# Optimization experiments

Hardware: AMD Instinct MI355X
Metric: run time of the kernel (lower is better)

The kernel has to match this reference:

```python
import jax, jax.numpy as jnp
import numpy as np

N = 8192
LATENT_DIM = 64


def setup_inputs() -> dict:
    key = jax.random.key(0)
    kx, ky = jax.random.split(key)
    x = jax.random.normal(kx, (N, LATENT_DIM), dtype=jnp.float32)
    y = jax.random.normal(ky, (N, LATENT_DIM), dtype=jnp.float32)
    return {"x": x, "y": y}


def _rbf_kernel(a, b):
    # Faithful to torch: exp(-mean((a_i - b_j)^2, axis=dim) / dim)
    #                  = exp(-||a_i - b_j||^2 / dim^2)
    # Computed via the expanded-sq-dist identity to avoid the [N, N, dim]
    # tiled intermediate the torch code materializes.
    dim = a.shape[1]
    sq_a = jnp.sum(a * a, axis=1)  # [Na]
    sq_b = jnp.sum(b * b, axis=1)  # [Nb]
    sq_dist = sq_a[:, None] + sq_b[None, :] - 2.0 * (a @ b.T)  # [Na, Nb]
    return jnp.exp(-sq_dist / (dim * dim))


def reference(x, y):
    # MMD with RBF kernel: mean k(x,x) + mean k(y,y) - 2 mean k(x,y)
    kxx = jnp.mean(_rbf_kernel(x, x))
    kyy = jnp.mean(_rbf_kernel(y, y))
    kxy = jnp.mean(_rbf_kernel(x, y))
    return kxx + kyy - 2.0 * kxy
```

## Files before the change

### kernel.cpp

```cpp
#include <hip/hip_runtime.h>
#include <cmath>

#define NPTS 8192
#define DIM 64
#define BT 128
#define KSTR 132

#define LEAF_F   0
#define LEAF_N   (3 * 8192 * 64)
#define ROWS_F   (LEAF_F + LEAF_N)
#define ROWS_N   (3 * 8192)
#define MEANS_F  (ROWS_F + ROWS_N)
#define NX_F     ((MEANS_F + 3 + 3) & ~3)
#define NY_F     (NX_F + 8192)
#define SPLIT_F  (NY_F + 8192)
#define SPLIT_ELEMS (NPTS * DIM)


typedef short bf16x8 __attribute__((ext_vector_type(8)));
typedef float f32x4  __attribute__((ext_vector_type(4)));

__device__ __forceinline__ unsigned short f32_bf16_rne(float f) {
    unsigned u = __float_as_uint(f);
    return (unsigned short)((u + 0x7FFFu + ((u >> 16) & 1u)) >> 16);
}
__device__ __forceinline__ float bf16_f32(unsigned short h) {
    return __uint_as_float(((unsigned)h) << 16);
}

__global__ void prep_kernel(const float* __restrict__ x, const float* __restrict__ y,
                            unsigned short* __restrict__ Xh, unsigned short* __restrict__ Xl,
                            unsigned short* __restrict__ Yh, unsigned short* __restrict__ Yl,
                            float* __restrict__ nx, float* __restrict__ ny) {
    int r = blockIdx.x * 256 + threadIdx.x;
    int isY = r >= NPTS;
    int rr = isY ? r - NPTS : r;
    const float4* Rg = (const float4*)((isY ? y : x) + (size_t)rr * DIM);
    unsigned short* Hh = isY ? Yh : Xh;
    unsigned short* Hl = isY ? Yl : Xl;
    const int t16 = rr >> 4, mrow = rr & 15;
    float s = 0.f;
    #pragma unroll
    for (int k4 = 0; k4 < 16; ++k4) {
        float4 v = Rg[k4];
        ushort4 h, l;
        h.x = f32_bf16_rne(v.x); l.x = f32_bf16_rne(v.x - bf16_f32(h.x));
        h.y = f32_bf16_rne(v.y); l.y = f32_bf16_rne(v.y - bf16_f32(h.y));
        h.z = f32_bf16_rne(v.z); l.z = f32_bf16_rne(v.z - bf16_f32(h.z));
        h.w = f32_bf16_rne(v.w); l.w = f32_bf16_rne(v.w - bf16_f32(h.w));
        int off = t16 * 1024 + (k4 >> 3) * 512 + ((k4 >> 1) & 3) * 128 + mrow * 8 + (k4 & 1) * 4;
        *(ushort4*)(Hh + off) = h;
        *(ushort4*)(Hl + off) = l;
        s = fmaf(v.x, v.x, s); s = fmaf(v.y, v.y, s);
        s = fmaf(v.z, v.z, s); s = fmaf(v.w, v.w, s);
    }
    if (isY) ny[rr] = s; else nx[rr] = s;
}

__global__ __launch_bounds__(512, 4) void mmd_tile_kernel(
    const unsigned short* __restrict__ Xh, const unsigned short* __restrict__ Xl,
    const unsigned short* __restrict__ Yh, const unsigned short* __restrict__ Yl,
    const float* __restrict__ nx, const float* __restrict__ ny,
    float* __restrict__ leafs)
{
    const int gi = blockIdx.x;
    const int gj = blockIdx.y;
    int zz, bx, by;
    if (blockIdx.z == 1) {
        if (gi >= 64) return;
        zz = 2; bx = gi; by = gj;
    } else if (gi > gj) {
        zz = 0; by = gj; bx = gi - 1;
    } else {
        zz = 1; by = gi; bx = gj;
    }

    __shared__ float Ks[128 * KSTR];
    __shared__ float sqA[BT];
    __shared__ float sqB[BT];

    const int t = threadIdx.x;
    const size_t arow = (size_t)by * BT;
    const size_t brow = (size_t)bx * BT;
    const int cb = bx;

    const unsigned short* pAh = (zz == 1) ? Yh : Xh;
    const unsigned short* pAl = (zz == 1) ? Yl : Xl;
    const unsigned short* pBh = (zz == 0) ? Xh : Yh;
    const unsigned short* pBl = (zz == 0) ? Xl : Yl;

    if (t < 256) {
        const float* nA = (zz == 1) ? ny : nx;
        const float* nB = (zz == 0) ? nx : ny;
        if (t < BT) sqA[t] = nA[arow + t];
        else        sqB[t - BT] = nB[brow + t - BT];
    }
    __syncthreads();

    const int lane = t & 63;
    const int wv   = t >> 6;
    const int mrow = lane & 15;
    const int quad = lane >> 4;
    const int rblk = (wv & 3) << 5;
    const int cblk = (wv >> 2) << 6;

    const int aT = by * 8 + (wv & 3) * 2;
    const int bT = bx * 8 + (wv >> 2) * 4;
    const int lsub = quad * 128 + mrow * 8;

    bf16x8 fAh[2][2], fAl[2][2];
    #pragma unroll
    for (int rt = 0; rt < 2; ++rt)
        #pragma unroll
        for (int kc = 0; kc < 2; ++kc) {
            int off = (aT + rt) * 1024 + kc * 512 + lsub;
            fAh[rt][kc] = *(const bf16x8*)(pAh + off);
            fAl[rt][kc] = *(const bf16x8*)(pAl + off);
        }

    f32x4 acc[2][4];
    #pragma unroll
    for (int rt = 0; rt < 2; ++rt)
        #pragma unroll
        for (int ct = 0; ct < 4; ++ct)
            acc[rt][ct] = (f32x4){0.f, 0.f, 0.f, 0.f};

    #pragma unroll
    for (int ct = 0; ct < 4; ++ct) {
        int boff = (bT + ct) * 1024 + lsub;
        bf16x8 bh0 = *(const bf16x8*)(pBh + boff);
        bf16x8 bh1 = *(const bf16x8*)(pBh + boff + 512);
        bf16x8 bl0 = *(const bf16x8*)(pBl + boff);
        bf16x8 bl1 = *(const bf16x8*)(pBl + boff + 512);
        #pragma unroll
        for (int rt = 0; rt < 2; ++rt) {
            f32x4 c = acc[rt][ct];
            c = __builtin_amdgcn_mfma_f32_16x16x32_bf16(fAh[rt][0], bh0, c, 0, 0, 0);
            c = __builtin_amdgcn_mfma_f32_16x16x32_bf16(fAh[rt][0], bl0, c, 0, 0, 0);
            c = __builtin_amdgcn_mfma_f32_16x16x32_bf16(fAl[rt][0], bh0, c, 0, 0, 0);
            c = __builtin_amdgcn_mfma_f32_16x16x32_bf16(fAh[rt][1], bh1, c, 0, 0, 0);
            c = __builtin_amdgcn_mfma_f32_16x16x32_bf16(fAh[rt][1], bl1, c, 0, 0, 0);
            c = __builtin_amdgcn_mfma_f32_16x16x32_bf16(fAl[rt][1], bh1, c, 0, 0, 0);
            acc[rt][ct] = c;
        }
    }

    const float SCL = (float)(-1.4426950408889634 / 4096.0);
    #pragma unroll
    for (int rt = 0; rt < 2; ++rt)
        #pragma unroll
        for (int ct = 0; ct < 4; ++ct)
            #pragma unroll
            for (int i = 0; i < 4; ++i) {
                int row = rblk + rt * 16 + quad * 4 + i;
                int col = cblk + ct * 16 + mrow;
                float d  = acc[rt][ct][i];
                float s2 = sqA[row] + sqB[col];
                float sqd = s2 - 2.0f * d;
                Ks[row * KSTR + col] = exp2f(sqd * SCL);
            }
    __syncthreads();

    float leaf[2];
    #pragma unroll
    for (int j = 0; j < 2; ++j) {
        int ch  = t + 512 * j;
        int row = ch >> 3;
        int tt  = ch & 7;
        float s = Ks[row * KSTR + tt];
        #pragma unroll
        for (int q = 1; q < 16; ++q) s += Ks[row * KSTR + tt + 8 * q];
        float p;
        p = __shfl_xor(s, 1); s = s + p;
        p = __shfl_xor(s, 2); s = s + p;
        p = __shfl_xor(s, 4); s = s + p;
        leaf[j] = s;
    }
    if ((t & 7) == 0) {
        int rb = t >> 3;
        #pragma unroll
        for (int j = 0; j < 2; ++j) {
            int row = rb + 64 * j;
            leafs[((size_t)zz * 8192 + arow + row) * 64 + cb] = leaf[j];
        }
    }

    if (zz < 2 && bx > by) {
        float mleaf[2];
        #pragma unroll
        for (int j = 0; j < 2; ++j) {
            int ch  = t + 512 * j;
            int c   = ch >> 3;
            int tt  = ch & 7;
            float s = Ks[tt * KSTR + c];
            #pragma unroll
            for (int q = 1; q < 16; ++q) s += Ks[(tt + 8 * q) * KSTR + c];
            float p;
            p = __shfl_xor(s, 1); s = s + p;
            p = __shfl_xor(s, 2); s = s + p;
            p = __shfl_xor(s, 4); s = s + p;
            mleaf[j] = s;
        }
        if ((t & 7) == 0) {
            int rb = t >> 3;
            #pragma unroll
            for (int j = 0; j < 2; ++j) {
                int row = rb + 64 * j;
                leafs[((size_t)zz * 8192 + brow + row) * 64 + by] = mleaf[j];
            }
        }
    }
}

__global__ void rowsum_kernel(const float* __restrict__ leafs, float* __restrict__ rowsums) {
    int tid = blockIdx.x * 256 + threadIdx.x;
    const float4* p = (const float4*)(leafs + (size_t)tid * 64);
    float v[64];
    #pragma unroll
    for (int i = 0; i < 16; ++i) {
        float4 q = p[i];
        v[4*i+0] = q.x; v[4*i+1] = q.y; v[4*i+2] = q.z; v[4*i+3] = q.w;
    }
    #pragma unroll
    for (int n = 32; n >= 1; n >>= 1)
        #pragma unroll
        for (int i = 0; i < 64; ++i)
            if (i < n) v[i] = v[2*i] + v[2*i+1];
    rowsums[tid] = v[0];
}

__global__ void colsum_kernel(const float* __restrict__ rowsums, float* __restrict__ means) {
    __shared__ float L[256];
    const int z = blockIdx.x;
    const int t = threadIdx.x;
    const float4* src = (const float4*)(rowsums + z * 8192);
    float v[32];
    #pragma unroll
    for (int i = 0; i < 8; ++i) {
        float4 q = src[t * 8 + i];
        v[4*i+0] = q.x; v[4*i+1] = q.y; v[4*i+2] = q.z; v[4*i+3] = q.w;
    }
    #pragma unroll
    for (int n = 16; n >= 1; n >>= 1)
        #pragma unroll
        for (int i = 0; i < 32; ++i)
            if (i < n) v[i] = v[2*i] + v[2*i+1];
    L[t] = v[0];
    __syncthreads();
    for (int n = 128; n >= 1; n >>= 1) {
        float w = 0.f;
        if (t < n) w = L[2*t] + L[2*t+1];
        __syncthreads();
        if (t < n) L[t] = w;
        __syncthreads();
    }
    if (t == 0) means[z] = L[0] * (1.0f / 67108864.0f);
}

__global__ void combine_kernel(const float* __restrict__ means, float* __restrict__ out) {
    float t1 = means[0] + means[1];
    out[0] = t1 - 2.0f * means[2];
}

extern "C" void kernel_launch(void* const* d_in, const int* in_sizes, int n_in,
                              void* d_out, int out_size, void* d_ws, size_t ws_size,
                              hipStream_t stream) {
    const float* x = (const float*)d_in[0];
    const float* y = (const float*)d_in[1];
    float* wsf     = (float*)d_ws;
    float* leafs   = wsf + LEAF_F;
    float* rowsums = wsf + ROWS_F;
    float* means   = wsf + MEANS_F;
    float* nx      = wsf + NX_F;
    float* ny      = wsf + NY_F;
    unsigned short* Xh = (unsigned short*)(wsf + SPLIT_F);
    unsigned short* Xl = Xh + SPLIT_ELEMS;
    unsigned short* Yh = Xl + SPLIT_ELEMS;
    unsigned short* Yl = Yh + SPLIT_ELEMS;

    prep_kernel<<<64, 256, 0, stream>>>(x, y, Xh, Xl, Yh, Yl, nx, ny);
    dim3 grid(65, 64, 2);
    mmd_tile_kernel<<<grid, 512, 0, stream>>>(Xh, Xl, Yh, Yl, nx, ny, leafs);
    rowsum_kernel<<<(3 * 8192) / 256, 256, 0, stream>>>(leafs, rowsums);
    colsum_kernel<<<3, 256, 0, stream>>>(rowsums, means);
    combine_kernel<<<1, 1, 0, stream>>>(means, (float*)d_out);
}
```

Baseline: 156.4 us.

## Fuse rowsum, colsum and combine into one last-block reduction kernel

```diff
diff --git a/kernel.cpp b/kernel.cpp
--- a/kernel.cpp
+++ b/kernel.cpp
@@ -11,7 +11,8 @@
 #define ROWS_F   (LEAF_F + LEAF_N)
 #define ROWS_N   (3 * 8192)
 #define MEANS_F  (ROWS_F + ROWS_N)
-#define NX_F     ((MEANS_F + 3 + 3) & ~3)
+#define CNT_F    (MEANS_F + 3)
+#define NX_F     ((CNT_F + 1 + 3) & ~3)
 #define NY_F     (NX_F + 8192)
 #define SPLIT_F  (NY_F + 8192)
 #define SPLIT_ELEMS (NPTS * DIM)
@@ -31,8 +32,10 @@
 __global__ void prep_kernel(const float* __restrict__ x, const float* __restrict__ y,
                             unsigned short* __restrict__ Xh, unsigned short* __restrict__ Xl,
                             unsigned short* __restrict__ Yh, unsigned short* __restrict__ Yl,
-                            float* __restrict__ nx, float* __restrict__ ny) {
-    int r = blockIdx.x * 256 + threadIdx.x;
+                            float* __restrict__ nx, float* __restrict__ ny,
+                            unsigned* __restrict__ cnt) {
+    int r = blockIdx.x * 64 + threadIdx.x;
+    if (r == 0) *cnt = 0u;
     int isY = r >= NPTS;
     int rr = isY ? r - NPTS : r;
     const float4* Rg = (const float4*)((isY ? y : x) + (size_t)rr * DIM);
@@ -181,7 +184,7 @@
         #pragma unroll
         for (int j = 0; j < 2; ++j) {
             int row = rb + 64 * j;
-            leafs[((size_t)zz * 8192 + arow + row) * 64 + cb] = leaf[j];
+            leafs[((size_t)zz * 64 + cb) * 8192 + arow + row] = leaf[j];
         }
     }
 
@@ -206,60 +209,71 @@
             #pragma unroll
             for (int j = 0; j < 2; ++j) {
                 int row = rb + 64 * j;
-                leafs[((size_t)zz * 8192 + brow + row) * 64 + by] = mleaf[j];
+                leafs[((size_t)zz * 64 + by) * 8192 + brow + row] = mleaf[j];
             }
         }
     }
 }
 
-__global__ void rowsum_kernel(const float* __restrict__ leafs, float* __restrict__ rowsums) {
-    int tid = blockIdx.x * 256 + threadIdx.x;
-    const float4* p = (const float4*)(leafs + (size_t)tid * 64);
+__global__ void reduce_kernel(const float* __restrict__ leafs, float* __restrict__ rowsums,
+                              unsigned* __restrict__ cnt, float* __restrict__ out) {
+    __shared__ float L[256];
+    __shared__ float M[3];
+    __shared__ int lastFlag;
+    const int t = threadIdx.x;
+    const int tid = blockIdx.x * 256 + t;
+    const int z = tid >> 13;
+    const int r = tid & 8191;
+
+    const float* base = leafs + ((size_t)z * 64) * 8192 + r;
     float v[64];
     #pragma unroll
-    for (int i = 0; i < 16; ++i) {
-        float4 q = p[i];
-        v[4*i+0] = q.x; v[4*i+1] = q.y; v[4*i+2] = q.z; v[4*i+3] = q.w;
-    }
+    for (int cbi = 0; cbi < 64; ++cbi) v[cbi] = base[(size_t)cbi * 8192];
     #pragma unroll
     for (int n = 32; n >= 1; n >>= 1)
         #pragma unroll
         for (int i = 0; i < 64; ++i)
             if (i < n) v[i] = v[2*i] + v[2*i+1];
     rowsums[tid] = v[0];
-}
-
-__global__ void colsum_kernel(const float* __restrict__ rowsums, float* __restrict__ means) {
-    __shared__ float L[256];
-    const int z = blockIdx.x;
-    const int t = threadIdx.x;
-    const float4* src = (const float4*)(rowsums + z * 8192);
-    float v[32];
-    #pragma unroll
-    for (int i = 0; i < 8; ++i) {
-        float4 q = src[t * 8 + i];
-        v[4*i+0] = q.x; v[4*i+1] = q.y; v[4*i+2] = q.z; v[4*i+3] = q.w;
-    }
-    #pragma unroll
-    for (int n = 16; n >= 1; n >>= 1)
-        #pragma unroll
-        for (int i = 0; i < 32; ++i)
-            if (i < n) v[i] = v[2*i] + v[2*i+1];
-    L[t] = v[0];
+
+    __threadfence();
+    if (t == 0) {
+        unsigned old = atomicAdd(cnt, 1u);
+        lastFlag = (old == 95u) ? 1 : 0;
+    }
     __syncthreads();
-    for (int n = 128; n >= 1; n >>= 1) {
-        float w = 0.f;
-        if (t < n) w = L[2*t] + L[2*t+1];
+    if (!lastFlag) return;
+    __threadfence();
+
+    for (int zz = 0; zz < 3; ++zz) {
+        const float4* src = (const float4*)(rowsums + zz * 8192);
+        float w[32];
+        #pragma unroll
+        for (int i = 0; i < 8; ++i) {
+            float4 q = src[t * 8 + i];
+            w[4*i+0] = q.x; w[4*i+1] = q.y; w[4*i+2] = q.z; w[4*i+3] = q.w;
+        }
+        #pragma unroll
+        for (int n = 16; n >= 1; n >>= 1)
+            #pragma unroll
+            for (int i = 0; i < 32; ++i)
+                if (i < n) w[i] = w[2*i] + w[2*i+1];
+        L[t] = w[0];
         __syncthreads();
-        if (t < n) L[t] = w;
+        for (int n = 128; n >= 1; n >>= 1) {
+            float u = 0.f;
+            if (t < n) u = L[2*t] + L[2*t+1];
+            __syncthreads();
+            if (t < n) L[t] = u;
+            __syncthreads();
+        }
+        if (t == 0) M[zz] = L[0] * (1.0f / 67108864.0f);
         __syncthreads();
     }
-    if (t == 0) means[z] = L[0] * (1.0f / 67108864.0f);
-}
-
-__global__ void combine_kernel(const float* __restrict__ means, float* __restrict__ out) {
-    float t1 = means[0] + means[1];
-    out[0] = t1 - 2.0f * means[2];
+    if (t == 0) {
+        float t1 = M[0] + M[1];
+        out[0] = t1 - 2.0f * M[2];
+    }
 }
 
 extern "C" void kernel_launch(void* const* d_in, const int* in_sizes, int n_in,
@@ -270,7 +284,7 @@
     float* wsf     = (float*)d_ws;
     float* leafs   = wsf + LEAF_F;
     float* rowsums = wsf + ROWS_F;
-    float* means   = wsf + MEANS_F;
+    unsigned* cnt  = (unsigned*)(wsf + CNT_F);
     float* nx      = wsf + NX_F;
     float* ny      = wsf + NY_F;
     unsigned short* Xh = (unsigned short*)(wsf + SPLIT_F);
@@ -278,10 +292,8 @@
     unsigned short* Yh = Xl + SPLIT_ELEMS;
     unsigned short* Yl = Yh + SPLIT_ELEMS;
 
-    prep_kernel<<<64, 256, 0, stream>>>(x, y, Xh, Xl, Yh, Yl, nx, ny);
+    prep_kernel<<<256, 64, 0, stream>>>(x, y, Xh, Xl, Yh, Yl, nx, ny, cnt);
     dim3 grid(65, 64, 2);
     mmd_tile_kernel<<<grid, 512, 0, stream>>>(Xh, Xl, Yh, Yl, nx, ny, leafs);
-    rowsum_kernel<<<(3 * 8192) / 256, 256, 0, stream>>>(leafs, rowsums);
-    colsum_kernel<<<3, 256, 0, stream>>>(rowsums, means);
-    combine_kernel<<<1, 1, 0, stream>>>(means, (float*)d_out);
-}
+    reduce_kernel<<<96, 256, 0, stream>>>(leafs, rowsums, cnt, (float*)d_out);
+}
```

New measurement: 160.7 us. +2.7%, slower.
